# Kernel optimization log

Hardware: AMD Instinct MI355X
Metric: run time of the kernel (lower is better)

The kernel has to match this reference:

```python
import jax, jax.numpy as jnp
import numpy as np

GENE_DIM = 3008   # conf.gene_dim
H = 6             # conf.num_hiddens_genotype (per-term hidden dim)
D_MODEL = 768     # conf.d_model
B = 4096          # batch
SIZES = [2048, 512, 128, 32, 8, 1]   # terms per topological layer (leaves -> root)
GPL = 8           # direct genes per leaf term
EPS = 1e-5        # BatchNorm1d eps


def setup_inputs() -> dict:
    key = jax.random.key(0)
    keys = iter(jax.random.split(key, 64))

    def rn(shape, scale=0.05):
        return jax.random.normal(next(keys), shape, dtype=jnp.float32) * scale

    inp = {"x": jax.random.normal(next(keys), (B, GENE_DIM), dtype=jnp.float32)}
    # batched per-leaf direct_gene_layer: Linear(GENE_DIM, GPL) for each leaf term
    inp["Wg"] = rn((SIZES[0], GPL, GENE_DIM))
    inp["bg"] = rn((SIZES[0], GPL))
    # per-layer term linear + batchnorm params; input sizes per layer
    in_sizes = [GPL, 4 * H, 4 * H, 4 * H, 4 * H, 8 * H]
    for i, (t, c) in enumerate(zip(SIZES, in_sizes)):
        inp[f"W{i}"] = rn((t, H, c))
        inp[f"b{i}"] = rn((t, H))
        inp[f"gm{i}"] = jnp.ones((t, H), jnp.float32)
        inp[f"bt{i}"] = jnp.zeros((t, H), jnp.float32)
    inp["Wf"] = rn((D_MODEL, H))
    inp["bf"] = rn((D_MODEL,))
    return inp


def _term_layer(child, W, b, gm, bt):
    # child: [B, T, in] ; W: [T, H, in] -> per-term Linear + tanh + BatchNorm1d(train)
    h = jnp.tanh(jnp.einsum('bti,toi->bto', child, W) + b)
    mu = h.mean(axis=0)              # [T, H] batch stats (biased var, as torch BN)
    var = h.var(axis=0)
    return (h - mu) * jax.lax.rsqrt(var + EPS) * gm + bt


def reference(x, Wg, bg,
              W0, b0, gm0, bt0, W1, b1, gm1, bt1, W2, b2, gm2, bt2,
              W3, b3, gm3, bt3, W4, b4, gm4, bt4, W5, b5, gm5, bt5,
              Wf, bf):
    gene = x[:, :GENE_DIM].astype(jnp.float32)        # x.narrow(1, 0, gene_dim)
    # all leaf direct_gene_layers batched: [B, T0, GPL]
    g = jnp.einsum('bg,tog->bto', gene, Wg) + bg
    h = _term_layer(g, W0, b0, gm0, bt0)              # leaf term layer: [B, T0, H]
    layer_params = [(W1, b1, gm1, bt1), (W2, b2, gm2, bt2), (W3, b3, gm3, bt3),
                    (W4, b4, gm4, bt4), (W5, b5, gm5, bt5)]
    for (W, b, gm, bt), T in zip(layer_params, SIZES[1:]):
        # gather-concat of child term outputs: contiguous fanout blocks -> reshape
        child = h.reshape(h.shape[0], T, -1)          # [B, T, fanout*H]
        h = _term_layer(child, W, b, gm, bt)
    root = h[:, 0, :]                                 # [B, H]
    return root @ Wf.T + bf                           # final_linear_layer -> [B, D_MODEL]
```

## Files before the change

### kernel.cpp

```cpp
#include <hip/hip_runtime.h>


typedef float f32x4 __attribute__((ext_vector_type(4)));
typedef __bf16 bf16x8 __attribute__((ext_vector_type(8)));

#define GL2LDS(g, l)                                                          \
  __builtin_amdgcn_global_load_lds(                                           \
      (__attribute__((address_space(1))) void*)(g),                           \
      (__attribute__((address_space(3))) void*)(l), 16, 0, 0)

__device__ __forceinline__ unsigned short f2bf(float f) {
  unsigned int u = __float_as_uint(f);
  u = u + 0x7fffu + ((u >> 16) & 1u);
  return (unsigned short)(u >> 16);
}

__device__ __forceinline__ float bf2f(unsigned int lo16) {
  return __uint_as_float(lo16 << 16);
}

__device__ __forceinline__ float tanh_fast(float x) {
  float e = __expf(2.0f * x);
  return 1.0f - __fdividef(2.0f, e + 1.0f);
}

__global__ __launch_bounds__(256) void cvt_all(
    const float* __restrict__ x, const float* __restrict__ wg,
    unsigned short* __restrict__ xb, unsigned short* __restrict__ wgb) {
  constexpr int NX = 12320768 / 4;
  constexpr int NW = 49283072 / 4;
  int i = blockIdx.x * 256 + threadIdx.x;
  const float* src;
  unsigned short* dst;
  int j;
  if (i < NX) {
    src = x; dst = xb; j = i;
  } else {
    j = i - NX;
    if (j >= NW) return;
    src = wg; dst = wgb;
  }
  float4 v = ((const float4*)src)[j];
  ushort4 o;
  o.x = f2bf(v.x); o.y = f2bf(v.y); o.z = f2bf(v.z); o.w = f2bf(v.w);
  ((ushort4*)dst)[j] = o;
}

__global__ __launch_bounds__(256, 2) void gemm_bt(
    const unsigned short* __restrict__ A, const unsigned short* __restrict__ Bm,
    const float* __restrict__ bias, unsigned short* __restrict__ C) {
  constexpr int N = 16384, K = 3008;
  __shared__ unsigned short As[128 * 64];
  __shared__ unsigned short Bs[128 * 64];
  const int tid = threadIdx.x;
  const int w = tid >> 6, l = tid & 63;
  const int m0 = blockIdx.y * 128, n0 = blockIdx.x * 128;

  const int srow = tid >> 3;
  const int cs = (tid & 7) ^ (srow & 7);
  const unsigned short* gA = A + (size_t)(m0 + srow) * K + cs * 8;
  const unsigned short* gB = Bm + (size_t)(n0 + srow) * K + cs * 8;
  unsigned short* lA = As + w * 512;
  unsigned short* lB = Bs + w * 512;

  f32x4 acc[4][4];
#pragma unroll
  for (int i = 0; i < 4; ++i)
#pragma unroll
    for (int j = 0; j < 4; ++j) acc[i][j] = (f32x4)0.0f;

  const int quad = l >> 4;
  const int lrow = l & 15;
  const int wm = (w >> 1) * 64, wn = (w & 1) * 64;

  for (int k0 = 0; k0 < K; k0 += 64) {
#pragma unroll
    for (int j = 0; j < 4; ++j) {
      GL2LDS(gA + (size_t)j * 32 * K + k0, lA + j * 2048);
      GL2LDS(gB + (size_t)j * 32 * K + k0, lB + j * 2048);
    }
    __syncthreads();
#pragma unroll
    for (int kk = 0; kk < 2; ++kk) {
      bf16x8 av[4], bv[4];
#pragma unroll
      for (int f = 0; f < 4; ++f) {
        int ra = wm + f * 16 + lrow;
        int ca = (kk * 4 + quad) ^ (ra & 7);
        av[f] = *(const bf16x8*)(As + ra * 64 + ca * 8);
        int rb = wn + f * 16 + lrow;
        int cb = (kk * 4 + quad) ^ (rb & 7);
        bv[f] = *(const bf16x8*)(Bs + rb * 64 + cb * 8);
      }
#pragma unroll
      for (int fm = 0; fm < 4; ++fm)
#pragma unroll
        for (int fn = 0; fn < 4; ++fn)
          acc[fm][fn] = __builtin_amdgcn_mfma_f32_16x16x32_bf16(
              av[fm], bv[fn], acc[fm][fn], 0, 0, 0);
    }
    __syncthreads();
  }

#pragma unroll
  for (int fn = 0; fn < 4; ++fn) {
    int n = n0 + wn + fn * 16 + lrow;
    float bn = bias[n];
#pragma unroll
    for (int fm = 0; fm < 4; ++fm) {
      int mbase = m0 + wm + fm * 16 + quad * 4;
#pragma unroll
      for (int r = 0; r < 4; ++r) {
        float v = acc[fm][fn][r] + bn;
        C[(size_t)(mbase + r) * N + n] = f2bf(v);
      }
    }
  }
}

template <int IC>
__device__ __forceinline__ void load_row(const unsigned short* p, float* d) {
  static_assert(IC % 8 == 0, "");
#pragma unroll
  for (int i = 0; i < IC / 8; ++i) {
    uint4 u = *(const uint4*)(p + i * 8);
    d[i * 8 + 0] = bf2f(u.x & 0xffffu); d[i * 8 + 1] = bf2f(u.x >> 16);
    d[i * 8 + 2] = bf2f(u.y & 0xffffu); d[i * 8 + 3] = bf2f(u.y >> 16);
    d[i * 8 + 4] = bf2f(u.z & 0xffffu); d[i * 8 + 5] = bf2f(u.z >> 16);
    d[i * 8 + 6] = bf2f(u.w & 0xffffu); d[i * 8 + 7] = bf2f(u.w >> 16);
  }
}
template <int IC>
__device__ __forceinline__ void load_row(const float* p, float* d) {
  static_assert(IC % 4 == 0, "");
#pragma unroll
  for (int i = 0; i < IC / 4; ++i) {
    float4 v = *(const float4*)(p + i * 4);
    d[i * 4 + 0] = v.x; d[i * 4 + 1] = v.y;
    d[i * 4 + 2] = v.z; d[i * 4 + 3] = v.w;
  }
}

template <typename TIN, typename TOUT, int T, int IC, int TG, bool FIRST>
__global__ __launch_bounds__(256) void term_layer(
    const TIN* __restrict__ in, const float* __restrict__ prevStats,
    const float* __restrict__ prevGm, const float* __restrict__ prevBt,
    const float* __restrict__ W, const float* __restrict__ bvec,
    TOUT* __restrict__ out, float* __restrict__ curStats) {
  constexpr int WIN = T * IC;
  constexpr int WOUT = T * 6;
  constexpr int NB = 256 / TG;
  const int tb = blockIdx.x * TG;
  const int t = threadIdx.x & (TG - 1);
  const int bsub = threadIdx.x / TG;

  __shared__ float sW[TG * 6 * IC];
  __shared__ float sB[TG * 6];
  __shared__ float sScale[FIRST ? 1 : TG * IC];
  __shared__ float sShift[FIRST ? 1 : TG * IC];
  __shared__ float sRed[256][13];

  for (int i = threadIdx.x; i < TG * 6 * IC; i += 256)
    sW[i] = W[(size_t)tb * 6 * IC + i];
  for (int i = threadIdx.x; i < TG * 6; i += 256) sB[i] = bvec[tb * 6 + i];
  if constexpr (!FIRST) {
    for (int i = threadIdx.x; i < TG * IC; i += 256) {
      int gc = tb * IC + i;
      float mu = prevStats[gc] * (1.0f / 4096.0f);
      float var = prevStats[WIN + gc] * (1.0f / 4096.0f) - mu * mu;
      float sc = rsqrtf(var + 1e-5f) * prevGm[gc];
      sScale[i] = sc;
      sShift[i] = prevBt[gc] - mu * sc;
    }
  }
  __syncthreads();

  float ls[6], lq[6];
#pragma unroll
  for (int i = 0; i < 6; ++i) { ls[i] = 0.0f; lq[i] = 0.0f; }

  const int bchunk = 4096 / gridDim.y;
  const int rows = bchunk / NB;
  const int b0 = blockIdx.y * bchunk + bsub * rows;
  for (int i = 0; i < rows; ++i) {
    int b = b0 + i;
    float child[IC];
    load_row<IC>(in + (size_t)b * WIN + (size_t)(tb + t) * IC, child);
    if constexpr (!FIRST) {
#pragma unroll
      for (int c = 0; c < IC; ++c)
        child[c] = child[c] * sScale[t * IC + c] + sShift[t * IC + c];
    }
    float hv[6];
#pragma unroll
    for (int o = 0; o < 6; ++o) {
      float a = sB[t * 6 + o];
      const float* wr = &sW[(t * 6 + o) * IC];
#pragma unroll
      for (int j = 0; j < IC; ++j) a += child[j] * wr[j];
      float h = tanh_fast(a);
      hv[o] = h;
      ls[o] += h;
      lq[o] += h * h;
    }
    TOUT* op = out + (size_t)b * WOUT + (size_t)(tb + t) * 6;
    if constexpr (sizeof(TOUT) == 2) {
      unsigned int* oi = (unsigned int*)op;
#pragma unroll
      for (int i2 = 0; i2 < 3; ++i2)
        oi[i2] = (unsigned int)f2bf(hv[2 * i2]) |
                 ((unsigned int)f2bf(hv[2 * i2 + 1]) << 16);
    } else {
#pragma unroll
      for (int i2 = 0; i2 < 6; ++i2) op[i2] = hv[i2];
    }
  }

#pragma unroll
  for (int j = 0; j < 6; ++j) {
    sRed[threadIdx.x][j] = ls[j];
    sRed[threadIdx.x][6 + j] = lq[j];
  }
  __syncthreads();
  for (int i = threadIdx.x; i < TG * 6; i += 256) {
    int tt = i / 6, o = i % 6;
    float s = 0.0f, q = 0.0f;
    for (int nb = 0; nb < NB; ++nb) {
      s += sRed[nb * TG + tt][o];
      q += sRed[nb * TG + tt][6 + o];
    }
    atomicAdd(&curStats[(tb + tt) * 6 + o], s);
    atomicAdd(&curStats[WOUT + (tb + tt) * 6 + o], q);
  }
}

__global__ __launch_bounds__(256) void final_fc(
    const float* __restrict__ h5, const float* __restrict__ stats5,
    const float* __restrict__ gm5, const float* __restrict__ bt5,
    const float* __restrict__ Wf, const float* __restrict__ bfv,
    float* __restrict__ out) {
  __shared__ float sWf[768 * 6];
  __shared__ float sbf[768];
  __shared__ float sRoot[8][6];
  const int tid = threadIdx.x;
  for (int i = tid; i < 768 * 6; i += 256) sWf[i] = Wf[i];
  for (int i = tid; i < 768; i += 256) sbf[i] = bfv[i];
  const int b0 = blockIdx.x * 8;
  if (tid < 48) {
    int bb = tid / 6, o = tid % 6;
    float mu = stats5[o] * (1.0f / 4096.0f);
    float var = stats5[6 + o] * (1.0f / 4096.0f) - mu * mu;
    float sc = rsqrtf(var + 1e-5f) * gm5[o];
    sRoot[bb][o] = (h5[(size_t)(b0 + bb) * 6 + o] - mu) * sc + bt5[o];
  }
  __syncthreads();
#pragma unroll
  for (int bb = 0; bb < 8; ++bb) {
    float r0 = sRoot[bb][0], r1 = sRoot[bb][1], r2 = sRoot[bb][2];
    float r3 = sRoot[bb][3], r4 = sRoot[bb][4], r5 = sRoot[bb][5];
    for (int d = tid; d < 768; d += 256) {
      const float* wr = &sWf[d * 6];
      float a = sbf[d] + r0 * wr[0] + r1 * wr[1] + r2 * wr[2] +
                r3 * wr[3] + r4 * wr[4] + r5 * wr[5];
      out[(size_t)(b0 + bb) * 768 + d] = a;
    }
  }
}

extern "C" void kernel_launch(void* const* d_in, const int* in_sizes, int n_in,
                              void* d_out, int out_size, void* d_ws,
                              size_t ws_size, hipStream_t stream) {
  const float* x   = (const float*)d_in[0];
  const float* Wg  = (const float*)d_in[1];
  const float* bg  = (const float*)d_in[2];
  const float* W0  = (const float*)d_in[3];
  const float* b0v = (const float*)d_in[4];
  const float* gm0 = (const float*)d_in[5];
  const float* bt0 = (const float*)d_in[6];
  const float* W1  = (const float*)d_in[7];
  const float* b1v = (const float*)d_in[8];
  const float* gm1 = (const float*)d_in[9];
  const float* bt1 = (const float*)d_in[10];
  const float* W2  = (const float*)d_in[11];
  const float* b2v = (const float*)d_in[12];
  const float* gm2 = (const float*)d_in[13];
  const float* bt2 = (const float*)d_in[14];
  const float* W3  = (const float*)d_in[15];
  const float* b3v = (const float*)d_in[16];
  const float* gm3 = (const float*)d_in[17];
  const float* bt3 = (const float*)d_in[18];
  const float* W4  = (const float*)d_in[19];
  const float* b4v = (const float*)d_in[20];
  const float* gm4 = (const float*)d_in[21];
  const float* bt4 = (const float*)d_in[22];
  const float* W5  = (const float*)d_in[23];
  const float* b5v = (const float*)d_in[24];
  const float* gm5 = (const float*)d_in[25];
  const float* bt5 = (const float*)d_in[26];
  const float* Wf  = (const float*)d_in[27];
  const float* bfv = (const float*)d_in[28];

  char* ws = (char*)d_ws;
  unsigned short* Xb  = (unsigned short*)(ws + 0);
  unsigned short* Wgb = (unsigned short*)(ws + 24641536ULL);
  unsigned short* G   = (unsigned short*)(ws + 123207680ULL);
  unsigned short* h0  = (unsigned short*)(ws + 257425408ULL);
  unsigned short* h1  = (unsigned short*)(ws + 358088704ULL);
  unsigned short* h2  = (unsigned short*)(ws + 383254528ULL);
  float* h3 = (float*)(ws + 389545984ULL);
  float* h4 = (float*)(ws + 392691712ULL);
  float* h5 = (float*)(ws + 393478144ULL);
  float* stats = (float*)(ws + 393576448ULL);

  hipMemsetAsync(stats, 0, 131072, stream);

  cvt_all<<<dim3(60160), 256, 0, stream>>>(x, Wg, Xb, Wgb);

  gemm_bt<<<dim3(128, 32), 256, 0, stream>>>(Xb, Wgb, bg, G);

  term_layer<unsigned short, unsigned short, 2048, 8, 64, true>
      <<<dim3(32, 16), 256, 0, stream>>>(G, nullptr, nullptr, nullptr, W0, b0v,
                                         h0, stats + 0);
  term_layer<unsigned short, unsigned short, 512, 24, 32, false>
      <<<dim3(16, 32), 256, 0, stream>>>(h0, stats + 0, gm0, bt0, W1, b1v, h1,
                                         stats + 24576);
  term_layer<unsigned short, unsigned short, 128, 24, 32, false>
      <<<dim3(4, 64), 256, 0, stream>>>(h1, stats + 24576, gm1, bt1, W2, b2v,
                                        h2, stats + 30720);
  term_layer<unsigned short, float, 32, 24, 32, false>
      <<<dim3(1, 128), 256, 0, stream>>>(h2, stats + 30720, gm2, bt2, W3, b3v,
                                         h3, stats + 32256);
  term_layer<float, float, 8, 24, 8, false>
      <<<dim3(1, 64), 256, 0, stream>>>(h3, stats + 32256, gm3, bt3, W4, b4v,
                                        h4, stats + 32640);
  term_layer<float, float, 1, 48, 1, false>
      <<<dim3(1, 16), 256, 0, stream>>>(h4, stats + 32640, gm4, bt4, W5, b5v,
                                        h5, stats + 32736);

  final_fc<<<dim3(512), 256, 0, stream>>>(h5, stats + 32736, gm5, bt5, Wf, bfv,
                                          (float*)d_out);
}
```

Before: 930.1 us.

## Rewrite gene GEMM with 256x256 tiles and a 4-stage async LDS pipeline

After: 921.3 us. About the same (-0.9%).

```diff
diff --git a/kernel.cpp b/kernel.cpp
--- a/kernel.cpp
+++ b/kernel.cpp
@@ -46,72 +46,107 @@
   ((ushort4*)dst)[j] = o;
 }
 
-__global__ __launch_bounds__(256, 2) void gemm_bt(
+__global__ __launch_bounds__(512, 2) void gemm_bt(
     const unsigned short* __restrict__ A, const unsigned short* __restrict__ Bm,
     const float* __restrict__ bias, unsigned short* __restrict__ C) {
   constexpr int N = 16384, K = 3008;
-  __shared__ unsigned short As[128 * 64];
-  __shared__ unsigned short Bs[128 * 64];
+  constexpr int NT = K / 32;
+  __shared__ unsigned short lds[65536];
   const int tid = threadIdx.x;
   const int w = tid >> 6, l = tid & 63;
-  const int m0 = blockIdx.y * 128, n0 = blockIdx.x * 128;
-
-  const int srow = tid >> 3;
-  const int cs = (tid & 7) ^ (srow & 7);
-  const unsigned short* gA = A + (size_t)(m0 + srow) * K + cs * 8;
-  const unsigned short* gB = Bm + (size_t)(n0 + srow) * K + cs * 8;
-  unsigned short* lA = As + w * 512;
-  unsigned short* lB = Bs + w * 512;
-
-  f32x4 acc[4][4];
-#pragma unroll
-  for (int i = 0; i < 4; ++i)
-#pragma unroll
-    for (int j = 0; j < 4; ++j) acc[i][j] = (f32x4)0.0f;
+  const int m0 = blockIdx.y * 256, n0 = blockIdx.x * 256;
+
+  const int srt = tid >> 3;
+  const int u0 = (tid & 7) ^ (srt & 7);
+  const int r0 = 2 * srt + (u0 >> 2);
+  const int c0e = (u0 & 3) * 8;
+  const unsigned short* gA0 = A + (size_t)(m0 + r0) * K + c0e;
+  const unsigned short* gA1 = gA0 + (size_t)128 * K;
+  const unsigned short* gB0 = Bm + (size_t)(n0 + r0) * K + c0e;
+  const unsigned short* gB1 = gB0 + (size_t)128 * K;
+
+#define STAGE(bufi, tt)                                                       \
+  do {                                                                        \
+    const int kofs_ = (tt) * 32;                                              \
+    unsigned short* dA_ = lds + (bufi) * 8192 + w * 512;                      \
+    unsigned short* dB_ = lds + 32768 + (bufi) * 8192 + w * 512;              \
+    GL2LDS(gA0 + kofs_, dA_);                                                 \
+    GL2LDS(gA1 + kofs_, dA_ + 4096);                                          \
+    GL2LDS(gB0 + kofs_, dB_);                                                 \
+    GL2LDS(gB1 + kofs_, dB_ + 4096);                                          \
+  } while (0)
 
   const int quad = l >> 4;
   const int lrow = l & 15;
-  const int wm = (w >> 1) * 64, wn = (w & 1) * 64;
-
-  for (int k0 = 0; k0 < K; k0 += 64) {
-#pragma unroll
-    for (int j = 0; j < 4; ++j) {
-      GL2LDS(gA + (size_t)j * 32 * K + k0, lA + j * 2048);
-      GL2LDS(gB + (size_t)j * 32 * K + k0, lB + j * 2048);
-    }
-    __syncthreads();
-#pragma unroll
-    for (int kk = 0; kk < 2; ++kk) {
-      bf16x8 av[4], bv[4];
-#pragma unroll
-      for (int f = 0; f < 4; ++f) {
-        int ra = wm + f * 16 + lrow;
-        int ca = (kk * 4 + quad) ^ (ra & 7);
-        av[f] = *(const bf16x8*)(As + ra * 64 + ca * 8);
-        int rb = wn + f * 16 + lrow;
-        int cb = (kk * 4 + quad) ^ (rb & 7);
-        bv[f] = *(const bf16x8*)(Bs + rb * 64 + cb * 8);
-      }
-#pragma unroll
-      for (int fm = 0; fm < 4; ++fm)
-#pragma unroll
-        for (int fn = 0; fn < 4; ++fn)
-          acc[fm][fn] = __builtin_amdgcn_mfma_f32_16x16x32_bf16(
-              av[fm], bv[fn], acc[fm][fn], 0, 0, 0);
-    }
-    __syncthreads();
-  }
-
-#pragma unroll
-  for (int fn = 0; fn < 4; ++fn) {
-    int n = n0 + wn + fn * 16 + lrow;
+  const int wm = (w >> 2) * 128, wn = (w & 3) * 64;
+  int aOff[8], bOff[4];
+#pragma unroll
+  for (int f = 0; f < 8; ++f) {
+    int ra = wm + f * 16 + lrow;
+    int sr = ra >> 1;
+    int ch = (((ra & 1) << 2) | quad) ^ (sr & 7);
+    aOff[f] = sr * 64 + ch * 8;
+  }
+#pragma unroll
+  for (int nn = 0; nn < 4; ++nn) {
+    int rb = wn + nn * 16 + lrow;
+    int sr = rb >> 1;
+    int ch = (((rb & 1) << 2) | quad) ^ (sr & 7);
+    bOff[nn] = sr * 64 + ch * 8;
+  }
+
+  f32x4 acc[8][4];
+#pragma unroll
+  for (int f = 0; f < 8; ++f)
+#pragma unroll
+    for (int nn = 0; nn < 4; ++nn) acc[f][nn] = (f32x4)0.0f;
+
+#define KTILE(t_, VMSTR, DOSTAGE)                                             \
+  {                                                                           \
+    if (DOSTAGE) STAGE(((t_) + 3) & 3, (t_) + 3);                             \
+    asm volatile("s_waitcnt " VMSTR ::: "memory");                            \
+    __builtin_amdgcn_s_barrier();                                             \
+    __builtin_amdgcn_sched_barrier(0);                                        \
+    const unsigned short* pa_ = lds + ((t_) & 3) * 8192;                      \
+    const unsigned short* pb_ = lds + 32768 + ((t_) & 3) * 8192;              \
+    bf16x8 av[8], bv[4];                                                      \
+    _Pragma("unroll") for (int f = 0; f < 8; ++f)                             \
+        av[f] = *(const bf16x8*)(pa_ + aOff[f]);                              \
+    _Pragma("unroll") for (int nn = 0; nn < 4; ++nn)                          \
+        bv[nn] = *(const bf16x8*)(pb_ + bOff[nn]);                            \
+    __builtin_amdgcn_s_setprio(1);                                            \
+    _Pragma("unroll") for (int f = 0; f < 8; ++f)                             \
+      _Pragma("unroll") for (int nn = 0; nn < 4; ++nn)                        \
+          acc[f][nn] = __builtin_amdgcn_mfma_f32_16x16x32_bf16(               \
+              av[f], bv[nn], acc[f][nn], 0, 0, 0);                            \
+    __builtin_amdgcn_s_setprio(0);                                            \
+    asm volatile("s_waitcnt lgkmcnt(0)" ::: "memory");                        \
+    __builtin_amdgcn_sched_barrier(0);                                        \
+    __builtin_amdgcn_s_barrier();                                             \
+  }
+
+  STAGE(0, 0);
+  STAGE(1, 1);
+  STAGE(2, 2);
+
+  for (int t = 0; t < NT - 3; ++t) KTILE(t, "vmcnt(12)", true);
+  KTILE(NT - 3, "vmcnt(8)", false);
+  KTILE(NT - 2, "vmcnt(4)", false);
+  KTILE(NT - 1, "vmcnt(0)", false);
+
+#undef KTILE
+#undef STAGE
+
+#pragma unroll
+  for (int nn = 0; nn < 4; ++nn) {
+    int n = n0 + wn + nn * 16 + lrow;
     float bn = bias[n];
 #pragma unroll
-    for (int fm = 0; fm < 4; ++fm) {
-      int mbase = m0 + wm + fm * 16 + quad * 4;
+    for (int f = 0; f < 8; ++f) {
+      int mbase = m0 + wm + f * 16 + quad * 4;
 #pragma unroll
       for (int r = 0; r < 4; ++r) {
-        float v = acc[fm][fn][r] + bn;
+        float v = acc[f][nn][r] + bn;
         C[(size_t)(mbase + r) * N + n] = f2bf(v);
       }
     }
@@ -316,17 +351,17 @@
 
   cvt_all<<<dim3(60160), 256, 0, stream>>>(x, Wg, Xb, Wgb);
 
-  gemm_bt<<<dim3(128, 32), 256, 0, stream>>>(Xb, Wgb, bg, G);
+  gemm_bt<<<dim3(64, 16), 512, 0, stream>>>(Xb, Wgb, bg, G);
 
   term_layer<unsigned short, unsigned short, 2048, 8, 64, true>
-      <<<dim3(32, 16), 256, 0, stream>>>(G, nullptr, nullptr, nullptr, W0, b0v,
+      <<<dim3(32, 64), 256, 0, stream>>>(G, nullptr, nullptr, nullptr, W0, b0v,
                                          h0, stats + 0);
   term_layer<unsigned short, unsigned short, 512, 24, 32, false>
-      <<<dim3(16, 32), 256, 0, stream>>>(h0, stats + 0, gm0, bt0, W1, b1v, h1,
+      <<<dim3(16, 64), 256, 0, stream>>>(h0, stats + 0, gm0, bt0, W1, b1v, h1,
                                          stats + 24576);
   term_layer<unsigned short, unsigned short, 128, 24, 32, false>
-      <<<dim3(4, 64), 256, 0, stream>>>(h1, stats + 24576, gm1, bt1, W2, b2v,
-                                        h2, stats + 30720);
+      <<<dim3(4, 128), 256, 0, stream>>>(h1, stats + 24576, gm1, bt1, W2, b2v,
+                                         h2, stats + 30720);
   term_layer<unsigned short, float, 32, 24, 32, false>
       <<<dim3(1, 128), 256, 0, stream>>>(h2, stats + 30720, gm2, bt2, W3, b3v,
                                          h3, stats + 32256);
```

## Rewrite gene GEMM as 256x256 double-buffered pipelined kernel; widen term-layer grids

Applied to the files above, without the earlier changes.

New measurement: 852.7 us. 8.3% less time.

```diff
diff --git a/kernel.cpp b/kernel.cpp
--- a/kernel.cpp
+++ b/kernel.cpp
@@ -46,73 +46,136 @@
   ((ushort4*)dst)[j] = o;
 }
 
-__global__ __launch_bounds__(256, 2) void gemm_bt(
+__global__ __launch_bounds__(512, 2) void gemm_bt(
     const unsigned short* __restrict__ A, const unsigned short* __restrict__ Bm,
     const float* __restrict__ bias, unsigned short* __restrict__ C) {
   constexpr int N = 16384, K = 3008;
-  __shared__ unsigned short As[128 * 64];
-  __shared__ unsigned short Bs[128 * 64];
+  __shared__ unsigned short lds[65536];
   const int tid = threadIdx.x;
   const int w = tid >> 6, l = tid & 63;
-  const int m0 = blockIdx.y * 128, n0 = blockIdx.x * 128;
-
-  const int srow = tid >> 3;
-  const int cs = (tid & 7) ^ (srow & 7);
-  const unsigned short* gA = A + (size_t)(m0 + srow) * K + cs * 8;
-  const unsigned short* gB = Bm + (size_t)(n0 + srow) * K + cs * 8;
-  unsigned short* lA = As + w * 512;
-  unsigned short* lB = Bs + w * 512;
-
-  f32x4 acc[4][4];
-#pragma unroll
-  for (int i = 0; i < 4; ++i)
+  const int m0 = blockIdx.y * 256, n0 = blockIdx.x * 256;
+
+  const int r0 = tid >> 3;
+  const int c0 = (tid & 7) ^ (r0 & 7);
+  const unsigned short* gA = A + (size_t)(m0 + r0) * K + c0 * 8;
+  const unsigned short* gB = Bm + (size_t)(n0 + r0) * K + c0 * 8;
+  const int wbase = w * 512;
+
+#define ASLOT(par, h) (lds + ((((par) << 1) | (h)) * 8192))
+#define BSLOT(par, h) (lds + 32768 + ((((par) << 1) | (h)) * 8192))
+
+#define STAGEA(par, h, kofE)                                                  \
+  do {                                                                        \
+    unsigned short* d_ = ASLOT(par, h) + wbase;                               \
+    GL2LDS(gA + (size_t)((h) * 128) * K + (kofE), d_);                        \
+    GL2LDS(gA + (size_t)((h) * 128 + 64) * K + (kofE), d_ + 4096);            \
+  } while (0)
+#define STAGEB(par, h, kofE)                                                  \
+  do {                                                                        \
+    unsigned short* d_ = BSLOT(par, h) + wbase;                               \
+    GL2LDS(gB + (size_t)((h) * 128) * K + (kofE), d_);                        \
+    GL2LDS(gB + (size_t)((h) * 128 + 64) * K + (kofE), d_ + 4096);            \
+  } while (0)
+
+  const int quad = l >> 4, lrow = l & 15;
+  int aO[2][4], bO[2][2];
+#pragma unroll
+  for (int f = 0; f < 4; ++f) {
+    int ra = (w >> 2) * 64 + f * 16 + lrow;
+#pragma unroll
+    for (int kk = 0; kk < 2; ++kk)
+      aO[kk][f] = ra * 64 + (((kk * 4 + quad) ^ (ra & 7)) * 8);
+  }
+#pragma unroll
+  for (int n = 0; n < 2; ++n) {
+    int rb = (w & 3) * 32 + n * 16 + lrow;
+#pragma unroll
+    for (int kk = 0; kk < 2; ++kk)
+      bO[kk][n] = rb * 64 + (((kk * 4 + quad) ^ (rb & 7)) * 8);
+  }
+
+  f32x4 acc[8][4];
+#pragma unroll
+  for (int i = 0; i < 8; ++i)
 #pragma unroll
     for (int j = 0; j < 4; ++j) acc[i][j] = (f32x4)0.0f;
-
-  const int quad = l >> 4;
-  const int lrow = l & 15;
-  const int wm = (w >> 1) * 64, wn = (w & 1) * 64;
-
-  for (int k0 = 0; k0 < K; k0 += 64) {
-#pragma unroll
-    for (int j = 0; j < 4; ++j) {
-      GL2LDS(gA + (size_t)j * 32 * K + k0, lA + j * 2048);
-      GL2LDS(gB + (size_t)j * 32 * K + k0, lB + j * 2048);
-    }
-    __syncthreads();
-#pragma unroll
-    for (int kk = 0; kk < 2; ++kk) {
-      bf16x8 av[4], bv[4];
-#pragma unroll
-      for (int f = 0; f < 4; ++f) {
-        int ra = wm + f * 16 + lrow;
-        int ca = (kk * 4 + quad) ^ (ra & 7);
-        av[f] = *(const bf16x8*)(As + ra * 64 + ca * 8);
-        int rb = wn + f * 16 + lrow;
-        int cb = (kk * 4 + quad) ^ (rb & 7);
-        bv[f] = *(const bf16x8*)(Bs + rb * 64 + cb * 8);
-      }
-#pragma unroll
-      for (int fm = 0; fm < 4; ++fm)
-#pragma unroll
-        for (int fn = 0; fn < 4; ++fn)
-          acc[fm][fn] = __builtin_amdgcn_mfma_f32_16x16x32_bf16(
-              av[fm], bv[fn], acc[fm][fn], 0, 0, 0);
-    }
-    __syncthreads();
-  }
-
-#pragma unroll
-  for (int fn = 0; fn < 4; ++fn) {
-    int n = n0 + wn + fn * 16 + lrow;
-    float bn = bias[n];
-#pragma unroll
-    for (int fm = 0; fm < 4; ++fm) {
-      int mbase = m0 + wm + fm * 16 + quad * 4;
+  bf16x8 av[4][2], bv[2][2];
+
+#define VM4 asm volatile("s_waitcnt vmcnt(4)" ::: "memory")
+#define VM0 asm volatile("s_waitcnt vmcnt(0)" ::: "memory")
+#define NOVM ((void)0)
+
+#define PHASE(par, mh, nh, LA, LB, STG, VMSTMT)                               \
+  {                                                                           \
+    if (LA) {                                                                 \
+      _Pragma("unroll") for (int f = 0; f < 4; ++f) {                         \
+        av[f][0] = *(const bf16x8*)(ASLOT(par, mh) + aO[0][f]);               \
+        av[f][1] = *(const bf16x8*)(ASLOT(par, mh) + aO[1][f]);               \
+      }                                                                       \
+    }                                                                         \
+    if (LB) {                                                                 \
+      _Pragma("unroll") for (int n = 0; n < 2; ++n) {                         \
+        bv[n][0] = *(const bf16x8*)(BSLOT(par, nh) + bO[0][n]);               \
+        bv[n][1] = *(const bf16x8*)(BSLOT(par, nh) + bO[1][n]);               \
+      }                                                                       \
+    }                                                                         \
+    STG;                                                                      \
+    VMSTMT;                                                                   \
+    __builtin_amdgcn_s_barrier();                                             \
+    asm volatile("s_waitcnt lgkmcnt(0)" ::: "memory");                        \
+    __builtin_amdgcn_sched_barrier(0);                                        \
+    __builtin_amdgcn_s_setprio(1);                                            \
+    _Pragma("unroll") for (int f = 0; f < 4; ++f)                             \
+      _Pragma("unroll") for (int n = 0; n < 2; ++n) {                         \
+        acc[(mh) * 4 + f][(nh) * 2 + n] =                                     \
+            __builtin_amdgcn_mfma_f32_16x16x32_bf16(                          \
+                av[f][0], bv[n][0], acc[(mh) * 4 + f][(nh) * 2 + n], 0, 0, 0);\
+        acc[(mh) * 4 + f][(nh) * 2 + n] =                                     \
+            __builtin_amdgcn_mfma_f32_16x16x32_bf16(                          \
+                av[f][1], bv[n][1], acc[(mh) * 4 + f][(nh) * 2 + n], 0, 0, 0);\
+      }                                                                       \
+    __builtin_amdgcn_s_setprio(0);                                            \
+    __builtin_amdgcn_s_barrier();                                             \
+  }
+
+#define STEP(par, S1, S2, VMSTMT)                                             \
+  PHASE(par, 0, 0, true, true, if (S1) STAGEA((par) ^ 1, 0, kof + 64), NOVM); \
+  PHASE(par, 1, 0, true, false, if (S1) STAGEB((par) ^ 1, 1, kof + 64), NOVM);\
+  PHASE(par, 1, 1, false, true, if (S2) STAGEB(par, 0, kof + 128), NOVM);     \
+  PHASE(par, 0, 1, true, false, if (S2) STAGEA(par, 1, kof + 128), VMSTMT);   \
+  kof += 64;
+
+  int kof = 0;
+  STAGEA(0, 0, 0); STAGEB(0, 0, 0); STAGEA(0, 1, 0); STAGEB(0, 1, 0);
+  STAGEB(1, 0, 64); STAGEA(1, 1, 64);
+  VM4;
+  __builtin_amdgcn_s_barrier();
+
+  for (int it = 0; it < 22; ++it) {
+    STEP(0, true, true, VM4);
+    STEP(1, true, true, VM4);
+  }
+  STEP(0, true, true, VM4);
+  STEP(1, true, false, VM0);
+  STEP(0, false, false, NOVM);
+
+#undef STEP
+#undef PHASE
+#undef STAGEA
+#undef STAGEB
+#undef ASLOT
+#undef BSLOT
+
+#pragma unroll
+  for (int bn = 0; bn < 4; ++bn) {
+    int n = n0 + (bn >> 1) * 128 + (w & 3) * 32 + (bn & 1) * 16 + lrow;
+    float bnv = bias[n];
+#pragma unroll
+    for (int F = 0; F < 8; ++F) {
+      int mbase = m0 + (F >> 2) * 128 + (w >> 2) * 64 + (F & 3) * 16 + quad * 4;
 #pragma unroll
       for (int r = 0; r < 4; ++r) {
-        float v = acc[fm][fn][r] + bn;
-        C[(size_t)(mbase + r) * N + n] = f2bf(v);
+        C[(size_t)(mbase + r) * N + n] = f2bf(acc[F][bn][r] + bnv);
       }
     }
   }
@@ -316,17 +379,17 @@
 
   cvt_all<<<dim3(60160), 256, 0, stream>>>(x, Wg, Xb, Wgb);
 
-  gemm_bt<<<dim3(128, 32), 256, 0, stream>>>(Xb, Wgb, bg, G);
+  gemm_bt<<<dim3(64, 16), 512, 0, stream>>>(Xb, Wgb, bg, G);
 
   term_layer<unsigned short, unsigned short, 2048, 8, 64, true>
-      <<<dim3(32, 16), 256, 0, stream>>>(G, nullptr, nullptr, nullptr, W0, b0v,
+      <<<dim3(32, 64), 256, 0, stream>>>(G, nullptr, nullptr, nullptr, W0, b0v,
                                          h0, stats + 0);
   term_layer<unsigned short, unsigned short, 512, 24, 32, false>
-      <<<dim3(16, 32), 256, 0, stream>>>(h0, stats + 0, gm0, bt0, W1, b1v, h1,
+      <<<dim3(16, 64), 256, 0, stream>>>(h0, stats + 0, gm0, bt0, W1, b1v, h1,
                                          stats + 24576);
   term_layer<unsigned short, unsigned short, 128, 24, 32, false>
-      <<<dim3(4, 64), 256, 0, stream>>>(h1, stats + 24576, gm1, bt1, W2, b2v,
-                                        h2, stats + 30720);
+      <<<dim3(4, 128), 256, 0, stream>>>(h1, stats + 24576, gm1, bt1, W2, b2v,
+                                         h2, stats + 30720);
   term_layer<unsigned short, float, 32, 24, 32, false>
       <<<dim3(1, 128), 256, 0, stream>>>(h2, stats + 30720, gm2, bt2, W3, b3v,
                                          h3, stats + 32256);
```
